# Kernel tuning notes

Hardware: AMD Instinct MI355X
Metric: run time of the kernel (lower is better)

Reference implementation:

```python
import jax, jax.numpy as jnp
import numpy as np

N = 100000          # num nodes
AVG_DEG = 16
E = N * AVG_DEG     # non-self-loop edges
D = 128             # in_dim == out_dim
H = 8               # heads
DH = D // H         # per-head dim
NEG_SLOPE = 0.2
EPS = 1e-5


def _layer_norm(h, g, b):
    mu = jnp.mean(h, axis=-1, keepdims=True)
    var = jnp.var(h, axis=-1, keepdims=True)
    return (h - mu) * jax.lax.rsqrt(var + EPS) * g + b


def setup_inputs() -> dict:
    key = jax.random.key(0)
    ks = jax.random.split(key, 12)
    x = jax.random.normal(ks[0], (N, D), dtype=jnp.float32)

    # edges with no self-loops, then append self-loops (mimics remove_self_loops + add_self_loops)
    rng = np.random.default_rng(0)
    src = rng.integers(0, N, size=E, dtype=np.int64)
    off = rng.integers(1, N, size=E, dtype=np.int64)
    dst = (src + off) % N
    loops = np.arange(N, dtype=np.int64)
    edge_index = jnp.asarray(
        np.stack([np.concatenate([src, loops]), np.concatenate([dst, loops])], axis=0))

    s = 0.02
    p = {
        'Wq': jax.random.normal(ks[1], (D, H * DH), jnp.float32) * s,
        'bq': jnp.zeros((H * DH,), jnp.float32),
        'Wk': jax.random.normal(ks[2], (D, H * DH), jnp.float32) * s,
        'bk': jnp.zeros((H * DH,), jnp.float32),
        'Wv': jax.random.normal(ks[3], (D, H * DH), jnp.float32) * s,
        'bv': jnp.zeros((H * DH,), jnp.float32),
        'Wo': jax.random.normal(ks[4], (D, D), jnp.float32) * s,
        'bo': jnp.zeros((D,), jnp.float32),
        'g1': jnp.ones((D,), jnp.float32),
        'b1': jnp.zeros((D,), jnp.float32),
        'Wf1': jax.random.normal(ks[5], (D, 2 * D), jnp.float32) * s,
        'bf1': jnp.zeros((2 * D,), jnp.float32),
        'Wf2': jax.random.normal(ks[6], (2 * D, D), jnp.float32) * s,
        'bf2': jnp.zeros((D,), jnp.float32),
        'g2': jnp.ones((D,), jnp.float32),
        'b2': jnp.zeros((D,), jnp.float32),
    }
    return {'x': x, 'edge_index': edge_index, **p}


def reference(x, edge_index, Wq, bq, Wk, bk, Wv, bv, Wo, bo, g1, b1,
              Wf1, bf1, Wf2, bf2, g2, b2):
    src, dst = edge_index[0], edge_index[1]

    Qh = (x @ Wq + bq).reshape(N, H, DH)
    Kh = (x @ Wk + bk).reshape(N, H, DH)
    Vh = (x @ Wv + bv).reshape(N, H, DH)

    # per-node scalar score per head: Q_n . K_n / sqrt(d_head)  -> [N, H]
    score = jnp.sum(Qh * Kh, axis=-1) / jnp.sqrt(jnp.float32(DH))

    # edge-wise: alpha = leaky_relu(score[src] + score[dst])  -> [Etot, H]
    alpha = jax.nn.leaky_relu(score[src] + score[dst], NEG_SLOPE)

    # segment softmax over destination nodes
    amax = jax.ops.segment_max(alpha, dst, num_segments=N)  # [N, H]
    ex = jnp.exp(alpha - amax[dst])
    denom = jax.ops.segment_sum(ex, dst, num_segments=N)
    alpha = ex / (denom[dst] + 1e-16)

    # weighted message aggregation: sum_j alpha_ij * V_j
    msg = Vh[src] * alpha[:, :, None]                        # [Etot, H, DH]
    out = jax.ops.segment_sum(msg, dst, num_segments=N)      # [N, H, DH]
    h = out.reshape(N, D)

    h = h @ Wo + bo
    h = h + x                       # residual 1
    h = _layer_norm(h, g1, b1)

    h2 = jax.nn.relu(h @ Wf1 + bf1)
    h2 = h2 @ Wf2 + bf2
    h = h2 + h                      # residual 2
    h = _layer_norm(h, g2, b2)
    return h
```

## Files before the change

### kernel.cpp

```cpp
#include <hip/hip_runtime.h>
#include <math.h>


#define GT_D 128

typedef short bf16x8 __attribute__((ext_vector_type(8)));
typedef float f32x4  __attribute__((ext_vector_type(4)));

union frag_u { bf16x8 v; ushort u[8]; };

__device__ __forceinline__ ushort f2bf(float f) {
    union { float f; unsigned u; } x; x.f = f;
    unsigned r = x.u + 0x7FFF + ((x.u >> 16) & 1);
    return (ushort)(r >> 16);
}
__device__ __forceinline__ float bf2f(ushort u) {
    union { unsigned u; float f; } x; x.u = ((unsigned)u) << 16; return x.f;
}

static inline char* align256(char* p) {
    return (char*)(((uintptr_t)p + 255) & ~(uintptr_t)255);
}

__global__ __launch_bounds__(256)
void ei_detect(const int* __restrict__ raw, int nOdd, int* __restrict__ flag)
{
    int i = blockIdx.x * 256 + threadIdx.x;
    int nz = 0;
    for (int j = i; j < nOdd; j += 256 * gridDim.x)
        nz |= (raw[2 * j + 1] != 0);
    if (nz) atomicOr(flag, 1);
}

__global__ __launch_bounds__(256)
void bucket_kernel(const int* __restrict__ raw, int Etot,
                   const int* __restrict__ flag,
                   int* __restrict__ deg, int* __restrict__ bucket)
{
    const int e = blockIdx.x * 256 + threadIdx.x;
    if (e >= Etot) return;
    const bool is64 = (*flag == 0);
    int s, d;
    if (is64) { s = raw[2 * e];  d = raw[2 * (Etot + e)]; }
    else      { s = raw[e];      d = raw[Etot + e]; }
    const int slot = atomicAdd(&deg[d], 1);
    if (slot < 64) bucket[(long)d * 64 + slot] = s;
}

__global__ __launch_bounds__(256)
void prep_qkv(const float* __restrict__ Wq, const float* __restrict__ Wk,
              const float* __restrict__ Wv, const float* __restrict__ bq,
              const float* __restrict__ bk, const float* __restrict__ bv,
              ushort* __restrict__ Wt, float* __restrict__ bias)
{
    const int i = blockIdx.x * 256 + threadIdx.x;
    if (i < 384 * 128) {
        const int n = i >> 7, k = i & 127;
        float v = (n < 128) ? Wq[k * 128 + n]
                : (n < 256) ? Wk[k * 128 + (n - 128)]
                            : Wv[k * 128 + (n - 256)];
        Wt[i] = f2bf(v);
    }
    if (i < 384)
        bias[i] = (i < 128) ? bq[i] : (i < 256) ? bk[i - 128] : bv[i - 256];
}

__global__ __launch_bounds__(256)
void prep_w(const float* __restrict__ W, ushort* __restrict__ Wt, int K, int N)
{
    const int i = blockIdx.x * 256 + threadIdx.x;
    if (i >= K * N) return;
    const int n = i / K, k = i - n * K;
    Wt[i] = f2bf(W[k * N + n]);
}

template<int MODE, bool AFP32, int CT>
__global__ __launch_bounds__(256)
void gemm_mfma(const void* __restrict__ Ap, int lda,
               const ushort* __restrict__ Wt, int K,
               const float* __restrict__ bias,
               const float* __restrict__ R, int ldr,
               void* __restrict__ Cp, int ldc, int M,
               float* __restrict__ scOut)
{
    const int w    = threadIdx.x >> 6;
    const int l    = threadIdx.x & 63;
    const int lr   = l & 15;
    const int lg   = l >> 4;
    const int row0 = blockIdx.x * 64 + w * 16;

    const int  arow  = row0 + lr;
    const long arowc = (arow < M) ? arow : (M - 1);

    f32x4 acc[CT];
    #pragma unroll
    for (int ct = 0; ct < CT; ++ct) acc[ct] = (f32x4){0.f, 0.f, 0.f, 0.f};

    for (int k0 = 0; k0 < K; k0 += 32) {
        frag_u a;
        if (AFP32) {
            const float* A = (const float*)Ap;
            const float4 f0 = *(const float4*)&A[arowc * lda + k0 + lg * 8];
            const float4 f1 = *(const float4*)&A[arowc * lda + k0 + lg * 8 + 4];
            a.u[0] = f2bf(f0.x); a.u[1] = f2bf(f0.y);
            a.u[2] = f2bf(f0.z); a.u[3] = f2bf(f0.w);
            a.u[4] = f2bf(f1.x); a.u[5] = f2bf(f1.y);
            a.u[6] = f2bf(f1.z); a.u[7] = f2bf(f1.w);
        } else {
            const ushort* A = (const ushort*)Ap;
            a.v = *(const bf16x8*)&A[arowc * lda + k0 + lg * 8];
        }
        #pragma unroll
        for (int ct = 0; ct < CT; ++ct) {
            const bf16x8 b = *(const bf16x8*)&Wt[(long)(ct * 16 + lr) * K + k0 + lg * 8];
            acc[ct] = __builtin_amdgcn_mfma_f32_16x16x32_bf16(a.v, b, acc[ct], 0, 0, 0);
        }
    }

    #pragma unroll
    for (int ct = 0; ct < CT; ++ct) {
        const float bv = bias[ct * 16 + lr];
        #pragma unroll
        for (int r = 0; r < 4; ++r) acc[ct][r] += bv;
    }

    if (MODE == 0) {
        #pragma unroll
        for (int h = 0; h < 8; ++h) {
            #pragma unroll
            for (int r = 0; r < 4; ++r) {
                float p = acc[h][r] * acc[h + 8][r];
                p += __shfl_xor(p, 1);
                p += __shfl_xor(p, 2);
                p += __shfl_xor(p, 4);
                p += __shfl_xor(p, 8);
                const int row = row0 + lg * 4 + r;
                if (lr == h && row < M) scOut[(long)row * 8 + h] = p * 0.25f;
            }
        }
        #pragma unroll
        for (int ct = 16; ct < 24; ++ct) {
            const int col = (ct - 16) * 16 + lr;
            #pragma unroll
            for (int r = 0; r < 4; ++r) {
                const int row = row0 + lg * 4 + r;
                if (row < M) ((ushort*)Cp)[(long)row * ldc + col] = f2bf(acc[ct][r]);
            }
        }
        return;
    }

    #pragma unroll
    for (int ct = 0; ct < CT; ++ct) {
        const int col = ct * 16 + lr;
        #pragma unroll
        for (int r = 0; r < 4; ++r) {
            const int row = row0 + lg * 4 + r;
            if (row >= M) continue;
            float v = acc[ct][r];
            if (MODE == 1) {
                v = v > 0.f ? v : 0.f;
                ((ushort*)Cp)[(long)row * ldc + col] = f2bf(v);
            } else {
                v += R[(long)row * ldr + col];
                ((float*)Cp)[(long)row * ldc + col] = v;
            }
        }
    }
}

__global__ __launch_bounds__(256)
void aggregate_kernel(const ushort* __restrict__ Z,
                      const float* __restrict__ score,
                      const int* __restrict__ deg,
                      const int* __restrict__ bucket,
                      int n)
{
    const int grp = threadIdx.x >> 5;
    const int l   = threadIdx.x & 31;
    const int d   = blockIdx.x * 8 + grp;
    if (d >= n) return;
    const int head   = l >> 2;
    const float sdst = score[(long)d * 8 + head];
    int dg = deg[d]; if (dg > 64) dg = 64;
    float psum = 0.f;
    float4 acc = make_float4(0.f, 0.f, 0.f, 0.f);
    for (int j = 0; j < dg; ++j) {
        const int s = bucket[(long)d * 64 + j];
        float a = score[(long)s * 8 + head] + sdst;
        a = a > 0.f ? a : 0.2f * a;
        const float p = __expf(a);
        psum += p;
        const ushort4 v = *(const ushort4*)&Z[(long)s * 256 + l * 4];
        acc.x += p * bf2f(v.x); acc.y += p * bf2f(v.y);
        acc.z += p * bf2f(v.z); acc.w += p * bf2f(v.w);
    }
    const float rinv = 1.0f / (psum + 1e-16f);
    ushort4 o;
    o.x = f2bf(acc.x * rinv); o.y = f2bf(acc.y * rinv);
    o.z = f2bf(acc.z * rinv); o.w = f2bf(acc.w * rinv);
    *(ushort4*)&((ushort*)Z)[(long)d * 256 + 128 + l * 4] = o;
}

__global__ __launch_bounds__(256)
void ln_kernel(const float* __restrict__ X, int ldx,
               const float* __restrict__ g, const float* __restrict__ b,
               float* __restrict__ outF, int ldo,
               ushort* __restrict__ outB, int ldob, int M)
{
    const int wave = threadIdx.x >> 6;
    const int lane = threadIdx.x & 63;
    const int row  = blockIdx.x * 4 + wave;
    if (row >= M) return;
    const float2 v = *(const float2*)&X[(long)row * ldx + lane * 2];
    float s = v.x + v.y;
    #pragma unroll
    for (int off = 32; off > 0; off >>= 1) s += __shfl_xor(s, off);
    const float mu = s * (1.0f / 128.0f);
    const float dx = v.x - mu, dy = v.y - mu;
    float q = dx * dx + dy * dy;
    #pragma unroll
    for (int off = 32; off > 0; off >>= 1) q += __shfl_xor(q, off);
    const float rstd = rsqrtf(q * (1.0f / 128.0f) + 1e-5f);
    const float2 gg = *(const float2*)&g[lane * 2];
    const float2 bb = *(const float2*)&b[lane * 2];
    float2 o;
    o.x = dx * rstd * gg.x + bb.x;
    o.y = dy * rstd * gg.y + bb.y;
    *(float2*)&outF[(long)row * ldo + lane * 2] = o;
    if (outB) {
        ushort2 ob; ob.x = f2bf(o.x); ob.y = f2bf(o.y);
        *(ushort2*)&outB[(long)row * ldob + lane * 2] = ob;
    }
}

extern "C" void kernel_launch(void* const* d_in, const int* in_sizes, int n_in,
                              void* d_out, int out_size, void* d_ws, size_t ws_size,
                              hipStream_t stream)
{
    const float* x   = (const float*)d_in[0];
    const int*   ei  = (const int*)d_in[1];
    const float* Wq  = (const float*)d_in[2];
    const float* bq  = (const float*)d_in[3];
    const float* Wk  = (const float*)d_in[4];
    const float* bk  = (const float*)d_in[5];
    const float* Wv  = (const float*)d_in[6];
    const float* bv  = (const float*)d_in[7];
    const float* Wo  = (const float*)d_in[8];
    const float* bo  = (const float*)d_in[9];
    const float* g1  = (const float*)d_in[10];
    const float* b1  = (const float*)d_in[11];
    const float* Wf1 = (const float*)d_in[12];
    const float* bf1 = (const float*)d_in[13];
    const float* Wf2 = (const float*)d_in[14];
    const float* bf2 = (const float*)d_in[15];
    const float* g2  = (const float*)d_in[16];
    const float* b2  = (const float*)d_in[17];
    float* out = (float*)d_out;

    const int N    = in_sizes[0] / GT_D;
    const int Etot = in_sizes[1] / 2;

    char* w = (char*)d_ws;
    ushort* Z     = (ushort*)w;  w = align256(w + (size_t)N * 256 * sizeof(ushort));
    float*  hp    = (float*)w;   w = align256(w + (size_t)N * 128 * sizeof(float));
    ushort* h1b   = (ushort*)w;  w = align256(w + (size_t)N * 128 * sizeof(ushort));
    float*  sc    = (float*)w;   w = align256(w + (size_t)N * 8 * sizeof(float));
    int*    deg   = (int*)w;     w = align256(w + (size_t)N * sizeof(int));
    int*    flag  = (int*)w;     w = align256(w + 256);
    int*    bkt   = (int*)w;     w = align256(w + (size_t)N * 64 * sizeof(int));
    ushort* wqkvt = (ushort*)w;  w = align256(w + (size_t)384 * 128 * sizeof(ushort));
    float*  bqkv  = (float*)w;   w = align256(w + 384 * sizeof(float));
    ushort* wot   = (ushort*)w;  w = align256(w + (size_t)128 * 128 * sizeof(ushort));
    ushort* wf1t  = (ushort*)w;  w = align256(w + (size_t)256 * 128 * sizeof(ushort));
    ushort* wf2t  = (ushort*)w;  w = align256(w + (size_t)128 * 256 * sizeof(ushort));
    float*  h1    = hp;
    ushort* att   = Z + 128;
    ushort* hid   = Z;

    const dim3 blk(256);
    const int mblk = (N + 63) / 64;

    hipMemsetAsync(flag, 0, sizeof(int), stream);
    hipMemsetAsync(deg, 0, (size_t)N * sizeof(int), stream);
    ei_detect<<<dim3(512), blk, 0, stream>>>(ei, Etot, flag);
    bucket_kernel<<<dim3((Etot + 255) / 256), blk, 0, stream>>>(ei, Etot, flag, deg, bkt);

    prep_qkv<<<dim3(192), blk, 0, stream>>>(Wq, Wk, Wv, bq, bk, bv, wqkvt, bqkv);
    prep_w<<<dim3(64),  blk, 0, stream>>>(Wo,  wot,  128, 128);
    prep_w<<<dim3(128), blk, 0, stream>>>(Wf1, wf1t, 128, 256);
    prep_w<<<dim3(128), blk, 0, stream>>>(Wf2, wf2t, 256, 128);

    gemm_mfma<0, true, 24><<<dim3(mblk), blk, 0, stream>>>(
        x, 128, wqkvt, 128, bqkv, nullptr, 0, Z, 256, N, sc);

    aggregate_kernel<<<dim3((N + 7) / 8), blk, 0, stream>>>(Z, sc, deg, bkt, N);

    gemm_mfma<2, false, 8><<<dim3(mblk), blk, 0, stream>>>(
        att, 256, wot, 128, bo, x, 128, hp, 128, N, nullptr);

    ln_kernel<<<dim3((N + 3) / 4), blk, 0, stream>>>(hp, 128, g1, b1, h1, 128, h1b, 128, N);

    gemm_mfma<1, false, 16><<<dim3(mblk), blk, 0, stream>>>(
        h1b, 128, wf1t, 128, bf1, nullptr, 0, hid, 256, N, nullptr);

    gemm_mfma<2, false, 8><<<dim3(mblk), blk, 0, stream>>>(
        hid, 256, wf2t, 256, bf2, h1, 128, out, 128, N, nullptr);

    ln_kernel<<<dim3((N + 3) / 4), blk, 0, stream>>>(out, 128, g2, b2, out, 128, nullptr, 0, N);
}
```

Before: 769.0 us.

## Hold weight fragments in registers and loop rows per block, splitting GEMMs by columns

Replaces the per-tile GEMM, which streamed weight fragments from global memory on every k-step, with kernels that load B fragments into registers once per block and reuse them across RT row tiles. Output columns are split across blockIdx.y so each block holds a smaller set of weight fragments. The QKV GEMM becomes two kernels: one computes only the Q/K per-head scores and one writes V. Keeping all fragments in registers raises register pressure. Splitting columns means the A rows are read again for each column split, and x is read twice in the QKV stage.

```diff
diff --git a/kernel.cpp b/kernel.cpp
--- a/kernel.cpp
+++ b/kernel.cpp
@@ -74,98 +74,161 @@
     Wt[i] = f2bf(W[k * N + n]);
 }
 
-template<int MODE, bool AFP32, int CT>
-__global__ __launch_bounds__(256)
-void gemm_mfma(const void* __restrict__ Ap, int lda,
-               const ushort* __restrict__ Wt, int K,
-               const float* __restrict__ bias,
-               const float* __restrict__ R, int ldr,
-               void* __restrict__ Cp, int ldc, int M,
-               float* __restrict__ scOut)
-{
-    const int w    = threadIdx.x >> 6;
-    const int l    = threadIdx.x & 63;
-    const int lr   = l & 15;
-    const int lg   = l >> 4;
-    const int row0 = blockIdx.x * 64 + w * 16;
-
-    const int  arow  = row0 + lr;
-    const long arowc = (arow < M) ? arow : (M - 1);
-
-    f32x4 acc[CT];
-    #pragma unroll
-    for (int ct = 0; ct < CT; ++ct) acc[ct] = (f32x4){0.f, 0.f, 0.f, 0.f};
-
-    for (int k0 = 0; k0 < K; k0 += 32) {
-        frag_u a;
-        if (AFP32) {
-            const float* A = (const float*)Ap;
-            const float4 f0 = *(const float4*)&A[arowc * lda + k0 + lg * 8];
-            const float4 f1 = *(const float4*)&A[arowc * lda + k0 + lg * 8 + 4];
-            a.u[0] = f2bf(f0.x); a.u[1] = f2bf(f0.y);
-            a.u[2] = f2bf(f0.z); a.u[3] = f2bf(f0.w);
-            a.u[4] = f2bf(f1.x); a.u[5] = f2bf(f1.y);
-            a.u[6] = f2bf(f1.z); a.u[7] = f2bf(f1.w);
-        } else {
-            const ushort* A = (const ushort*)Ap;
-            a.v = *(const bf16x8*)&A[arowc * lda + k0 + lg * 8];
+template<bool AFP32>
+__device__ __forceinline__ bf16x8 load_afrag(const void* Ap, long off)
+{
+    frag_u a;
+    if (AFP32) {
+        const float* A = (const float*)Ap;
+        const float4 f0 = *(const float4*)&A[off];
+        const float4 f1 = *(const float4*)&A[off + 4];
+        a.u[0] = f2bf(f0.x); a.u[1] = f2bf(f0.y);
+        a.u[2] = f2bf(f0.z); a.u[3] = f2bf(f0.w);
+        a.u[4] = f2bf(f1.x); a.u[5] = f2bf(f1.y);
+        a.u[6] = f2bf(f1.z); a.u[7] = f2bf(f1.w);
+    } else {
+        a.v = *(const bf16x8*)&((const ushort*)Ap)[off];
+    }
+    return a.v;
+}
+
+template<int MODE, bool AFP32, int CT, int KS, int RT>
+__global__ __launch_bounds__(256)
+void gemm_rowloop(const void* __restrict__ Ap, int lda,
+                  const ushort* __restrict__ Wt,
+                  const float* __restrict__ bias,
+                  const float* __restrict__ R, int ldr,
+                  void* __restrict__ Cp, int ldc, int M)
+{
+    constexpr int K = KS * 32;
+    const int w  = threadIdx.x >> 6;
+    const int l  = threadIdx.x & 63;
+    const int lr = l & 15;
+    const int lg = l >> 4;
+    const int colbase = blockIdx.y * (CT * 16);
+
+    bf16x8 bfr[KS][CT];
+    #pragma unroll
+    for (int ks = 0; ks < KS; ++ks)
+        #pragma unroll
+        for (int ct = 0; ct < CT; ++ct)
+            bfr[ks][ct] = *(const bf16x8*)
+                &Wt[(size_t)(colbase + ct * 16 + lr) * K + ks * 32 + lg * 8];
+
+    float bv[CT];
+    #pragma unroll
+    for (int ct = 0; ct < CT; ++ct) bv[ct] = bias[colbase + ct * 16 + lr];
+
+    #pragma unroll
+    for (int r = 0; r < RT; ++r) {
+        const int row0 = (blockIdx.x * RT + r) * 64 + w * 16;
+        const int arow = row0 + lr;
+        const long arowc = (arow < M) ? arow : (M - 1);
+
+        bf16x8 a[KS];
+        #pragma unroll
+        for (int ks = 0; ks < KS; ++ks)
+            a[ks] = load_afrag<AFP32>(Ap, arowc * (long)lda + ks * 32 + lg * 8);
+
+        f32x4 acc[CT];
+        #pragma unroll
+        for (int ct = 0; ct < CT; ++ct) acc[ct] = (f32x4){0.f, 0.f, 0.f, 0.f};
+        #pragma unroll
+        for (int ks = 0; ks < KS; ++ks)
+            #pragma unroll
+            for (int ct = 0; ct < CT; ++ct)
+                acc[ct] = __builtin_amdgcn_mfma_f32_16x16x32_bf16(
+                    a[ks], bfr[ks][ct], acc[ct], 0, 0, 0);
+
+        #pragma unroll
+        for (int ct = 0; ct < CT; ++ct) {
+            const int col = colbase + ct * 16 + lr;
+            #pragma unroll
+            for (int rr = 0; rr < 4; ++rr) {
+                const int row = row0 + lg * 4 + rr;
+                if (row >= M) continue;
+                float v = acc[ct][rr] + bv[ct];
+                if (MODE == 1) v = v > 0.f ? v : 0.f;
+                if (MODE == 0 || MODE == 1) {
+                    ((ushort*)Cp)[(size_t)row * ldc + col] = f2bf(v);
+                } else {
+                    v += R[(size_t)row * ldr + col];
+                    ((float*)Cp)[(size_t)row * ldc + col] = v;
+                }
+            }
         }
-        #pragma unroll
-        for (int ct = 0; ct < CT; ++ct) {
-            const bf16x8 b = *(const bf16x8*)&Wt[(long)(ct * 16 + lr) * K + k0 + lg * 8];
-            acc[ct] = __builtin_amdgcn_mfma_f32_16x16x32_bf16(a.v, b, acc[ct], 0, 0, 0);
+    }
+}
+
+template<int RT>
+__global__ __launch_bounds__(256)
+void gemm_qk_score(const float* __restrict__ A,
+                   const ushort* __restrict__ Wt,
+                   const float* __restrict__ bias,
+                   float* __restrict__ sc, int M)
+{
+    const int w  = threadIdx.x >> 6;
+    const int l  = threadIdx.x & 63;
+    const int lr = l & 15;
+    const int lg = l >> 4;
+    const int y  = blockIdx.y;
+    const int qcol = y * 64;
+    const int kcol = 128 + y * 64;
+
+    bf16x8 bq_[4][4], bk_[4][4];
+    #pragma unroll
+    for (int ks = 0; ks < 4; ++ks)
+        #pragma unroll
+        for (int ct = 0; ct < 4; ++ct) {
+            bq_[ks][ct] = *(const bf16x8*)
+                &Wt[(size_t)(qcol + ct * 16 + lr) * 128 + ks * 32 + lg * 8];
+            bk_[ks][ct] = *(const bf16x8*)
+                &Wt[(size_t)(kcol + ct * 16 + lr) * 128 + ks * 32 + lg * 8];
         }
-    }
-
-    #pragma unroll
-    for (int ct = 0; ct < CT; ++ct) {
-        const float bv = bias[ct * 16 + lr];
-        #pragma unroll
-        for (int r = 0; r < 4; ++r) acc[ct][r] += bv;
-    }
-
-    if (MODE == 0) {
-        #pragma unroll
-        for (int h = 0; h < 8; ++h) {
+    float bvq[4], bvk[4];
+    #pragma unroll
+    for (int ct = 0; ct < 4; ++ct) {
+        bvq[ct] = bias[qcol + ct * 16 + lr];
+        bvk[ct] = bias[kcol + ct * 16 + lr];
+    }
+
+    #pragma unroll
+    for (int r = 0; r < RT; ++r) {
+        const int row0 = (blockIdx.x * RT + r) * 64 + w * 16;
+        const int arow = row0 + lr;
+        const long arowc = (arow < M) ? arow : (M - 1);
+
+        bf16x8 a[4];
+        #pragma unroll
+        for (int ks = 0; ks < 4; ++ks)
+            a[ks] = load_afrag<true>(A, arowc * 128L + ks * 32 + lg * 8);
+
+        f32x4 aq[4], ak[4];
+        #pragma unroll
+        for (int ct = 0; ct < 4; ++ct) {
+            aq[ct] = (f32x4){0.f, 0.f, 0.f, 0.f};
+            ak[ct] = (f32x4){0.f, 0.f, 0.f, 0.f};
+        }
+        #pragma unroll
+        for (int ks = 0; ks < 4; ++ks)
             #pragma unroll
-            for (int r = 0; r < 4; ++r) {
-                float p = acc[h][r] * acc[h + 8][r];
+            for (int ct = 0; ct < 4; ++ct) {
+                aq[ct] = __builtin_amdgcn_mfma_f32_16x16x32_bf16(a[ks], bq_[ks][ct], aq[ct], 0, 0, 0);
+                ak[ct] = __builtin_amdgcn_mfma_f32_16x16x32_bf16(a[ks], bk_[ks][ct], ak[ct], 0, 0, 0);
+            }
+
+        #pragma unroll
+        for (int j = 0; j < 4; ++j)
+            #pragma unroll
+            for (int rr = 0; rr < 4; ++rr) {
+                float p = (aq[j][rr] + bvq[j]) * (ak[j][rr] + bvk[j]);
                 p += __shfl_xor(p, 1);
                 p += __shfl_xor(p, 2);
                 p += __shfl_xor(p, 4);
                 p += __shfl_xor(p, 8);
-                const int row = row0 + lg * 4 + r;
-                if (lr == h && row < M) scOut[(long)row * 8 + h] = p * 0.25f;
+                const int row = row0 + lg * 4 + rr;
+                if (lr == j && row < M) sc[(size_t)row * 8 + y * 4 + j] = p * 0.25f;
             }
-        }
-        #pragma unroll
-        for (int ct = 16; ct < 24; ++ct) {
-            const int col = (ct - 16) * 16 + lr;
-            #pragma unroll
-            for (int r = 0; r < 4; ++r) {
-                const int row = row0 + lg * 4 + r;
-                if (row < M) ((ushort*)Cp)[(long)row * ldc + col] = f2bf(acc[ct][r]);
-            }
-        }
-        return;
-    }
-
-    #pragma unroll
-    for (int ct = 0; ct < CT; ++ct) {
-        const int col = ct * 16 + lr;
-        #pragma unroll
-        for (int r = 0; r < 4; ++r) {
-            const int row = row0 + lg * 4 + r;
-            if (row >= M) continue;
-            float v = acc[ct][r];
-            if (MODE == 1) {
-                v = v > 0.f ? v : 0.f;
-                ((ushort*)Cp)[(long)row * ldc + col] = f2bf(v);
-            } else {
-                v += R[(long)row * ldr + col];
-                ((float*)Cp)[(long)row * ldc + col] = v;
-            }
-        }
     }
 }
 
@@ -279,7 +342,8 @@
     ushort* hid   = Z;
 
     const dim3 blk(256);
-    const int mblk = (N + 63) / 64;
+    const int RT = 2;
+    const int rblk = (N + 64 * RT - 1) / (64 * RT);
 
     hipMemsetAsync(flag, 0, sizeof(int), stream);
     hipMemsetAsync(deg, 0, (size_t)N * sizeof(int), stream);
@@ -291,21 +355,23 @@
     prep_w<<<dim3(128), blk, 0, stream>>>(Wf1, wf1t, 128, 256);
     prep_w<<<dim3(128), blk, 0, stream>>>(Wf2, wf2t, 256, 128);
 
-    gemm_mfma<0, true, 24><<<dim3(mblk), blk, 0, stream>>>(
-        x, 128, wqkvt, 128, bqkv, nullptr, 0, Z, 256, N, sc);
+    gemm_qk_score<2><<<dim3(rblk, 2), blk, 0, stream>>>(x, wqkvt, bqkv, sc, N);
+
+    gemm_rowloop<0, true, 8, 4, 2><<<dim3(rblk, 1), blk, 0, stream>>>(
+        x, 128, wqkvt + (size_t)256 * 128, bqkv + 256, nullptr, 0, Z, 256, N);
 
     aggregate_kernel<<<dim3((N + 7) / 8), blk, 0, stream>>>(Z, sc, deg, bkt, N);
 
-    gemm_mfma<2, false, 8><<<dim3(mblk), blk, 0, stream>>>(
-        att, 256, wot, 128, bo, x, 128, hp, 128, N, nullptr);
+    gemm_rowloop<2, false, 8, 4, 2><<<dim3(rblk, 1), blk, 0, stream>>>(
+        att, 256, wot, bo, x, 128, hp, 128, N);
 
     ln_kernel<<<dim3((N + 3) / 4), blk, 0, stream>>>(hp, 128, g1, b1, h1, 128, h1b, 128, N);
 
-    gemm_mfma<1, false, 16><<<dim3(mblk), blk, 0, stream>>>(
-        h1b, 128, wf1t, 128, bf1, nullptr, 0, hid, 256, N, nullptr);
-
-    gemm_mfma<2, false, 8><<<dim3(mblk), blk, 0, stream>>>(
-        hid, 256, wf2t, 256, bf2, h1, 128, out, 128, N, nullptr);
+    gemm_rowloop<1, false, 8, 4, 2><<<dim3(rblk, 2), blk, 0, stream>>>(
+        h1b, 128, wf1t, bf1, nullptr, 0, hid, 256, N);
+
+    gemm_rowloop<2, false, 4, 8, 2><<<dim3(rblk, 2), blk, 0, stream>>>(
+        hid, 256, wf2t, bf2, h1, 128, out, 128, N);
 
     ln_kernel<<<dim3((N + 3) / 4), blk, 0, stream>>>(out, 128, g2, b2, out, 128, nullptr, 0, N);
 }
```

Measured after the change: 706.2 us. -8.2%, faster.
